# Performance work log

Hardware: AMD Instinct MI355X
Metric: run time of the kernel (lower is better)

## Reference

```python
import jax, jax.numpy as jnp
import numpy as np

N_NODES = 100000
N_EDGES = 3200000


def gcn_conv(x, edge_index, W, b, n):
    # PyG GCNConv: h = x @ W; add self-loops; symmetric deg normalization; scatter-add; + bias
    src = edge_index[0]
    dst = edge_index[1]
    loop = jnp.arange(n, dtype=src.dtype)
    src = jnp.concatenate([src, loop])
    dst = jnp.concatenate([dst, loop])
    ones = jnp.ones(src.shape[0], dtype=x.dtype)
    deg = jax.ops.segment_sum(ones, dst, num_segments=n)  # in-degree with self-loops
    dinv = jnp.where(deg > 0, jax.lax.rsqrt(deg), 0.0)
    norm = dinv[src] * dinv[dst]  # [E+N]
    h = x @ W  # [N, out]
    msg = h[src] * norm[:, None]
    out = jax.ops.segment_sum(msg, dst, num_segments=n)
    return out + b


def setup_inputs() -> dict:
    key = jax.random.key(0)
    ks = jax.random.split(key, 8)
    x = jax.random.normal(ks[0], (N_NODES, 1024), dtype=jnp.float32)
    edge_index = jax.random.randint(ks[1], (2, N_EDGES), 0, N_NODES, dtype=jnp.int32)
    def glorot(k, fan_in, fan_out):
        s = jnp.sqrt(6.0 / (fan_in + fan_out))
        return jax.random.uniform(k, (fan_in, fan_out), jnp.float32, -s, s)
    W1 = glorot(ks[2], 1024, 128)
    W2 = glorot(ks[3], 128, 128)
    W3 = glorot(ks[4], 128, 9)
    b1 = jnp.zeros((128,), jnp.float32)
    b2 = jnp.zeros((128,), jnp.float32)
    b3 = jnp.zeros((9,), jnp.float32)
    return {"x": x, "edge_index": edge_index, "W1": W1, "b1": b1, "W2": W2, "b2": b2, "W3": W3, "b3": b3}


def reference(x, edge_index, W1, b1, W2, b2, W3, b3):
    n = x.shape[0]
    h = jax.nn.relu(gcn_conv(x, edge_index, W1, b1, n))
    h = jax.nn.relu(gcn_conv(h, edge_index, W2, b2, n))
    h = gcn_conv(h, edge_index, W3, b3, n)
    return jax.nn.log_softmax(h, axis=1)
```

## Files before the change

kernel.cpp:

```cpp
#include <hip/hip_runtime.h>
#include <hip/hip_bf16.h>

typedef __attribute__((ext_vector_type(8))) short bf16x8;
typedef __attribute__((ext_vector_type(4))) float f32x4;

#define BSH 8
#define BNODES 256

__device__ __forceinline__ unsigned short f2bf(float f) {
    union { float f; unsigned int u; } x; x.f = f;
    unsigned int u = x.u;
    unsigned int r = (u + 0x7fffu + ((u >> 16) & 1u)) >> 16;
    return (unsigned short)r;
}
__device__ __forceinline__ float bf_lo(unsigned int v) { return __uint_as_float(v << 16); }
__device__ __forceinline__ float bf_hi(unsigned int v) { return __uint_as_float(v & 0xffff0000u); }

__device__ __forceinline__ void gll16(const void* g, void* l) {
    __builtin_amdgcn_global_load_lds(
        (const __attribute__((address_space(1))) unsigned int*)g,
        (__attribute__((address_space(3))) unsigned int*)l, 16, 0, 0);
}

template <int N> __device__ __forceinline__ void waitvm() {
    if constexpr (N == 0) asm volatile("s_waitcnt vmcnt(0)" ::: "memory");
    else if constexpr (N == 4) asm volatile("s_waitcnt vmcnt(4)" ::: "memory");
    else if constexpr (N == 6) asm volatile("s_waitcnt vmcnt(6)" ::: "memory");
    else if constexpr (N == 8) asm volatile("s_waitcnt vmcnt(8)" ::: "memory");
    else if constexpr (N == 12) asm volatile("s_waitcnt vmcnt(12)" ::: "memory");
    else static_assert(N == 0, "unhandled vmcnt");
}


__global__ void k_zero(int* p, int n) {
    int i = blockIdx.x * 256 + threadIdx.x;
    if (i < n) p[i] = 0;
}

__global__ __launch_bounds__(256) void kA_hist(const int* __restrict__ dst, int* bhist,
                                               int E, int nbkt) {
    __shared__ int h[512];
    for (int i = threadIdx.x; i < 512; i += 256) h[i] = 0;
    __syncthreads();
    int stride = gridDim.x * 256;
    int n4 = E >> 2;
    for (int i = blockIdx.x * 256 + threadIdx.x; i < n4; i += stride) {
        int4 d = ((const int4*)dst)[i];
        atomicAdd(&h[d.x >> BSH], 1);
        atomicAdd(&h[d.y >> BSH], 1);
        atomicAdd(&h[d.z >> BSH], 1);
        atomicAdd(&h[d.w >> BSH], 1);
    }
    for (int i = (n4 << 2) + blockIdx.x * 256 + threadIdx.x; i < E; i += stride)
        atomicAdd(&h[dst[i] >> BSH], 1);
    __syncthreads();
    for (int i = threadIdx.x; i < nbkt; i += 256)
        if (h[i]) atomicAdd(&bhist[i], h[i]);
}

__global__ void kA_scan(const int* bhist, int* bbase, int* bcur, int nbkt) {
    __shared__ int s[512];
    int t = threadIdx.x;
    int v = (t < nbkt) ? bhist[t] : 0;
    s[t] = v;
    __syncthreads();
    for (int o = 1; o < 512; o <<= 1) {
        int x = (t >= o) ? s[t - o] : 0;
        __syncthreads();
        s[t] += x;
        __syncthreads();
    }
    if (t < nbkt) { bbase[t] = s[t] - v; bcur[t] = s[t] - v; }
    if (t == nbkt - 1) bbase[nbkt] = s[t];
}

#define TPE 16
__global__ __launch_bounds__(256) void kA_scatter(const int* __restrict__ src,
                                                  const int* __restrict__ dst,
                                                  int* bcur, unsigned int* pairs,
                                                  int E, int nbkt) {
    __shared__ int hist[512];
    __shared__ int base[512];
    const int tid = threadIdx.x;
    const int t0 = blockIdx.x * (256 * TPE);
    for (int i = tid; i < 512; i += 256) hist[i] = 0;
    __syncthreads();

    int es[TPE], ed[TPE], rk[TPE];
    bool valid[TPE];
    if (t0 + 256 * TPE <= E) {
        const int4* s4 = (const int4*)(src + t0 + tid * TPE);
        const int4* d4 = (const int4*)(dst + t0 + tid * TPE);
#pragma unroll
        for (int j = 0; j < TPE / 4; j++) {
            int4 a = s4[j], b = d4[j];
            es[4 * j + 0] = a.x; es[4 * j + 1] = a.y; es[4 * j + 2] = a.z; es[4 * j + 3] = a.w;
            ed[4 * j + 0] = b.x; ed[4 * j + 1] = b.y; ed[4 * j + 2] = b.z; ed[4 * j + 3] = b.w;
            valid[4 * j + 0] = valid[4 * j + 1] = valid[4 * j + 2] = valid[4 * j + 3] = true;
        }
    } else {
#pragma unroll
        for (int j = 0; j < TPE; j++) {
            int e = t0 + tid * TPE + j;
            valid[j] = (e < E);
            es[j] = valid[j] ? src[e] : 0;
            ed[j] = valid[j] ? dst[e] : 0;
        }
    }
#pragma unroll
    for (int j = 0; j < TPE; j++)
        if (valid[j]) rk[j] = atomicAdd(&hist[ed[j] >> BSH], 1);
    __syncthreads();
    for (int i = tid; i < nbkt; i += 256) {
        int c = hist[i];
        base[i] = c ? atomicAdd(&bcur[i], c) : 0;
    }
    __syncthreads();
#pragma unroll
    for (int j = 0; j < TPE; j++) {
        if (valid[j]) {
            int b = ed[j] >> BSH;
            unsigned int p = ((unsigned int)(ed[j] & (BNODES - 1)) << 24) | (unsigned int)es[j];
            pairs[base[b] + rk[j]] = p;
        }
    }
}

__global__ __launch_bounds__(512) void kB_group(const unsigned int* __restrict__ pairs,
                                                const int* __restrict__ bbase,
                                                int* csr, int* offs, int* cnt, float* dinv,
                                                int N, int nbkt) {
    int b = blockIdx.x;
    int p0 = bbase[b], p1 = bbase[b + 1];
    int node0 = b << BSH;
    int nn = min(BNODES, N - node0);
    __shared__ int lcnt[BNODES];
    __shared__ int ss[BNODES];
    __shared__ int lcur[BNODES];
    int t = threadIdx.x;
    if (t < BNODES) lcnt[t] = 0;
    __syncthreads();
    for (int i = p0 + t; i < p1; i += 512)
        atomicAdd(&lcnt[pairs[i] >> 24], 1);
    __syncthreads();
    int v = (t < BNODES) ? lcnt[t] : 0;
    if (t < BNODES) ss[t] = v;
    __syncthreads();
    for (int o = 1; o < BNODES; o <<= 1) {
        int x = (t >= o && t < BNODES) ? ss[t - o] : 0;
        __syncthreads();
        if (t < BNODES) ss[t] += x;
        __syncthreads();
    }
    if (t < nn) {
        int o = p0 + ss[t] - v;
        offs[node0 + t] = o;
        cnt[node0 + t] = v;
        dinv[node0 + t] = rsqrtf((float)(v + 1));
        lcur[t] = o;
    }
    __syncthreads();
    for (int i = p0 + t; i < p1; i += 512) {
        unsigned int p = pairs[i];
        int pos = atomicAdd(&lcur[p >> 24], 1);
        csr[pos] = (int)(p & 0xFFFFFFu);
    }
}

__global__ void k_wt2(const float* __restrict__ W1, unsigned short* w1t,
                      const float* __restrict__ W2, unsigned short* w2t) {
    int i = blockIdx.x * 256 + threadIdx.x;
    if (i < 1024 * 128) {
        int k = i >> 7, c = i & 127;
        w1t[c * 1024 + k] = f2bf(W1[i]);
    } else {
        int j = i - 1024 * 128;
        if (j < 128 * 128) {
            int k = j >> 7, c = j & 127;
            w2t[c * 128 + k] = f2bf(W2[j]);
        }
    }
}


template <int K, bool IN_F32>
__global__ __launch_bounds__(256) void k_gemm(const void* __restrict__ Xv,
                                              const unsigned short* __restrict__ Wt,
                                              const float* __restrict__ dinv,
                                              unsigned short* __restrict__ G, int M) {
    constexpr int ABYTES = IN_F32 ? 128 * 32 * 4 : 128 * 32 * 2;
    constexpr int BBYTES = 128 * 32 * 2;
    constexpr int NT = K / 32;
    constexpr int NBUF = 3;
    constexpr int L = IN_F32 ? 6 : 4;
    static_assert(NT >= 3, "pipeline needs >=3 tiles");
    __shared__ char smem[NBUF * (ABYTES + BBYTES)];

    const int tid = threadIdx.x;
    const int m0 = blockIdx.x * 128;
    const int w = tid >> 6, l = tid & 63, r = l & 15, kg = l >> 4;
    const int wb0 = tid & ~63;

    auto stage = [&](int buf, int k0) {
        if (IN_F32) {
            const float* X = (const float*)Xv;
            char* ab = smem + buf * ABYTES;
#pragma unroll
            for (int i = 0; i < 4; i++) {
                int wb = i * 256 + wb0;
                int c = wb + l;
                int row = c >> 3, slot = c & 7;
                int srow = m0 + row; if (srow >= M) srow = M - 1;
                gll16(X + (size_t)srow * K + k0 + slot * 4, ab + (size_t)wb * 16);
            }
        } else {
            const unsigned short* X = (const unsigned short*)Xv;
            char* ab = smem + buf * ABYTES;
#pragma unroll
            for (int i = 0; i < 2; i++) {
                int wb = i * 256 + wb0;
                int c = wb + l;
                int row = c >> 2, slot = c & 3;
                int srow = m0 + row; if (srow >= M) srow = M - 1;
                gll16(X + (size_t)srow * K + k0 + slot * 8, ab + (size_t)wb * 16);
            }
        }
        {
            char* bb = smem + NBUF * ABYTES + buf * BBYTES;
#pragma unroll
            for (int i = 0; i < 2; i++) {
                int wb = i * 256 + wb0;
                int c = wb + l;
                int row = c >> 2, slot = c & 3;
                gll16(Wt + (size_t)row * K + k0 + slot * 8, bb + (size_t)wb * 16);
            }
        }
    };

    f32x4 acc[2][8];
#pragma unroll
    for (int mt = 0; mt < 2; mt++)
#pragma unroll
        for (int ct = 0; ct < 8; ct++) acc[mt][ct] = (f32x4){0.f, 0.f, 0.f, 0.f};

    auto compute = [&](int buf) {
        bf16x8 af[2], bfr[8];
        if (IN_F32) {
            const float* ab = (const float*)(smem + buf * ABYTES);
#pragma unroll
            for (int mt = 0; mt < 2; mt++) {
                int row = w * 32 + mt * 16 + r;
                float4 f0 = *(const float4*)(ab + row * 32 + kg * 8);
                float4 f1 = *(const float4*)(ab + row * 32 + kg * 8 + 4);
                union { bf16x8 v; unsigned short u[8]; } a;
                a.u[0] = f2bf(f0.x); a.u[1] = f2bf(f0.y); a.u[2] = f2bf(f0.z); a.u[3] = f2bf(f0.w);
                a.u[4] = f2bf(f1.x); a.u[5] = f2bf(f1.y); a.u[6] = f2bf(f1.z); a.u[7] = f2bf(f1.w);
                af[mt] = a.v;
            }
        } else {
            const unsigned short* ab = (const unsigned short*)(smem + buf * ABYTES);
#pragma unroll
            for (int mt = 0; mt < 2; mt++) {
                int row = w * 32 + mt * 16 + r;
                af[mt] = *(const bf16x8*)(ab + row * 32 + kg * 8);
            }
        }
        {
            const unsigned short* bb = (const unsigned short*)(smem + NBUF * ABYTES + buf * BBYTES);
#pragma unroll
            for (int ct = 0; ct < 8; ct++)
                bfr[ct] = *(const bf16x8*)(bb + (ct * 16 + r) * 32 + kg * 8);
        }
#pragma unroll
        for (int mt = 0; mt < 2; mt++)
#pragma unroll
            for (int ct = 0; ct < 8; ct++)
                acc[mt][ct] = __builtin_amdgcn_mfma_f32_16x16x32_bf16(af[mt], bfr[ct], acc[mt][ct], 0, 0, 0);
    };

    stage(0, 0);
    stage(1, 32);

    int cur = 0;
    for (int t = 0; t < NT - 2; ++t) {
        int nb = cur + 2; if (nb >= NBUF) nb -= NBUF;
        waitvm<L>();
        __builtin_amdgcn_s_barrier();
        stage(nb, (t + 2) * 32);
        compute(cur);
        cur = (cur + 1 == NBUF) ? 0 : cur + 1;
    }
    waitvm<L>();
    __builtin_amdgcn_s_barrier();
    compute(cur);
    cur = (cur + 1 == NBUF) ? 0 : cur + 1;
    waitvm<0>();
    __builtin_amdgcn_s_barrier();
    compute(cur);

#pragma unroll
    for (int mt = 0; mt < 2; mt++) {
        int rbase = m0 + w * 32 + mt * 16 + kg * 4;
        float dv[4];
#pragma unroll
        for (int q = 0; q < 4; q++) dv[q] = (rbase + q < M) ? dinv[rbase + q] : 0.f;
#pragma unroll
        for (int ct = 0; ct < 8; ct++) {
#pragma unroll
            for (int q = 0; q < 4; q++) {
                int gr = rbase + q;
                if (gr < M) G[(size_t)gr * 128 + ct * 16 + r] = f2bf(acc[mt][ct][q] * dv[q]);
            }
        }
    }
}


__global__ __launch_bounds__(256) void k_gemm3(const unsigned short* X3, const float* W3,
                                               const float* dinv, unsigned short* G3, int M) {
    __shared__ unsigned short sx[128 * 136];
    __shared__ float sw[128 * 9];
    int tid = threadIdx.x;
    int m0 = blockIdx.x * 128;
#pragma unroll
    for (int p = 0; p < 8; p++) {
        int idx = p * 256 + tid;
        int row = idx >> 4, c8 = idx & 15;
        uint4 v = make_uint4(0u, 0u, 0u, 0u);
        if (m0 + row < M) v = *(const uint4*)(X3 + (size_t)(m0 + row) * 128 + c8 * 8);
        *(uint4*)&sx[row * 136 + c8 * 8] = v;
    }
    for (int i = tid; i < 128 * 9; i += 256) sw[i] = W3[i];
    __syncthreads();

    int r = tid >> 1, h = tid & 1;
    float acc[9];
#pragma unroll
    for (int c = 0; c < 9; c++) acc[c] = 0.f;
    for (int kk = 0; kk < 64; kk++) {
        int k = h * 64 + kk;
        float xv = __uint_as_float(((unsigned int)sx[r * 136 + k]) << 16);
#pragma unroll
        for (int c = 0; c < 9; c++) acc[c] += xv * sw[k * 9 + c];
    }
#pragma unroll
    for (int c = 0; c < 9; c++) acc[c] += __shfl_xor(acc[c], 1);
    int gr = m0 + r;
    if (h == 0 && gr < M) {
        float dv = dinv[gr];
#pragma unroll
        for (int c = 0; c < 9; c++) G3[(size_t)gr * 16 + c] = f2bf(acc[c] * dv);
#pragma unroll
        for (int c = 9; c < 16; c++) G3[(size_t)gr * 16 + c] = 0;
    }
}


#define A128_CAP 1024

__global__ __launch_bounds__(256) void k_agg128(const unsigned int* __restrict__ gv,
                                                const int* __restrict__ csr,
                                                const int* __restrict__ offs,
                                                const int* __restrict__ cnt,
                                                const float* __restrict__ dinv,
                                                const float* __restrict__ bias,
                                                unsigned int* xout, int N, int do_relu) {
    __shared__ int sidx[A128_CAP];
    const int tid = threadIdx.x;
    const int n0 = blockIdx.x * 4;
    const int nlast = min(n0 + 3, N - 1);
    const int base = offs[n0];
    const int tot = offs[nlast] + cnt[nlast] - base;
    const bool lds_ok = (tot <= A128_CAP);
    if (lds_ok)
        for (int i = tid; i < tot; i += 256) sidx[i] = csr[base + i];
    __syncthreads();

    const int node = n0 + (tid >> 6);
    if (node >= N) return;
    const int l = tid & 63;
    const int ne = cnt[node];
    const int st = offs[node] - base;

    unsigned int u = gv[node * 64 + l];
    float a0 = bf_lo(u), a1 = bf_hi(u);
    int e = 0;
    if (lds_ok) {
        for (; e + 8 <= ne; e += 8) {
            int s0 = sidx[st + e], s1 = sidx[st + e + 1];
            int s2 = sidx[st + e + 2], s3 = sidx[st + e + 3];
            int s4 = sidx[st + e + 4], s5 = sidx[st + e + 5];
            int s6 = sidx[st + e + 6], s7 = sidx[st + e + 7];
            unsigned int v0 = gv[s0 * 64 + l], v1 = gv[s1 * 64 + l];
            unsigned int v2 = gv[s2 * 64 + l], v3 = gv[s3 * 64 + l];
            unsigned int v4 = gv[s4 * 64 + l], v5 = gv[s5 * 64 + l];
            unsigned int v6 = gv[s6 * 64 + l], v7 = gv[s7 * 64 + l];
            a0 += bf_lo(v0); a1 += bf_hi(v0);
            a0 += bf_lo(v1); a1 += bf_hi(v1);
            a0 += bf_lo(v2); a1 += bf_hi(v2);
            a0 += bf_lo(v3); a1 += bf_hi(v3);
            a0 += bf_lo(v4); a1 += bf_hi(v4);
            a0 += bf_lo(v5); a1 += bf_hi(v5);
            a0 += bf_lo(v6); a1 += bf_hi(v6);
            a0 += bf_lo(v7); a1 += bf_hi(v7);
        }
        for (; e < ne; e++) {
            unsigned int v = gv[sidx[st + e] * 64 + l];
            a0 += bf_lo(v); a1 += bf_hi(v);
        }
    } else {
        const int gst = offs[node];
        for (; e < ne; e++) {
            unsigned int v = gv[csr[gst + e] * 64 + l];
            a0 += bf_lo(v); a1 += bf_hi(v);
        }
    }
    float dv = dinv[node];
    float o0 = fmaf(dv, a0, bias[2 * l]);
    float o1 = fmaf(dv, a1, bias[2 * l + 1]);
    if (do_relu) { o0 = fmaxf(o0, 0.f); o1 = fmaxf(o1, 0.f); }
    xout[node * 64 + l] = (unsigned int)f2bf(o0) | ((unsigned int)f2bf(o1) << 16);
}


#define A9_CAP 3072

__global__ __launch_bounds__(256) void k_agg9(const unsigned int* __restrict__ g3v,
                                              const int* __restrict__ csr,
                                              const int* __restrict__ offs,
                                              const int* __restrict__ cnt,
                                              const float* __restrict__ dinv,
                                              const float* __restrict__ b3,
                                              float* out, int N) {
    __shared__ int sidx[A9_CAP];
    const int tid = threadIdx.x;
    const int n0 = blockIdx.x * 32;
    const int nlast = min(n0 + 31, N - 1);
    const int base = offs[n0];
    const int tot = offs[nlast] + cnt[nlast] - base;
    const bool lds_ok = (tot <= A9_CAP);
    if (lds_ok)
        for (int i = tid; i < tot; i += 256) sidx[i] = csr[base + i];
    __syncthreads();

    const int node = n0 + (tid >> 3);
    if (node >= N) return;
    const int jl = tid & 7;
    const int ne = cnt[node];

    unsigned int u = g3v[node * 8 + jl];
    float a0 = bf_lo(u), a1 = bf_hi(u);
    int e = 0;
    if (lds_ok) {
        const int st = offs[node] - base;
        for (; e + 4 <= ne; e += 4) {
            int s0 = sidx[st + e], s1 = sidx[st + e + 1];
            int s2 = sidx[st + e + 2], s3 = sidx[st + e + 3];
            unsigned int v0 = g3v[s0 * 8 + jl], v1 = g3v[s1 * 8 + jl];
            unsigned int v2 = g3v[s2 * 8 + jl], v3 = g3v[s3 * 8 + jl];
            a0 += bf_lo(v0); a1 += bf_hi(v0);
            a0 += bf_lo(v1); a1 += bf_hi(v1);
            a0 += bf_lo(v2); a1 += bf_hi(v2);
            a0 += bf_lo(v3); a1 += bf_hi(v3);
        }
        for (; e < ne; e++) {
            unsigned int v = g3v[sidx[st + e] * 8 + jl];
            a0 += bf_lo(v); a1 += bf_hi(v);
        }
    } else {
        const int gst = offs[node];
        for (; e < ne; e++) {
            unsigned int v = g3v[csr[gst + e] * 8 + jl];
            a0 += bf_lo(v); a1 += bf_hi(v);
        }
    }
    float dv = dinv[node];
    int c0 = 2 * jl, c1 = 2 * jl + 1;
    float o0 = (c0 < 9) ? fmaf(dv, a0, b3[c0]) : -INFINITY;
    float o1 = (c1 < 9) ? fmaf(dv, a1, b3[c1]) : -INFINITY;
    float m = fmaxf(o0, o1);
    for (int d = 1; d < 8; d <<= 1) m = fmaxf(m, __shfl_xor(m, d));
    float s = 0.f;
    if (c0 < 9) s += expf(o0 - m);
    if (c1 < 9) s += expf(o1 - m);
    for (int d = 1; d < 8; d <<= 1) s += __shfl_xor(s, d);
    float ls = m + logf(s);
    if (c0 < 9) out[(size_t)node * 9 + c0] = o0 - ls;
    if (c1 < 9) out[(size_t)node * 9 + c1] = o1 - ls;
}


extern "C" void kernel_launch(void* const* d_in, const int* in_sizes, int n_in,
                              void* d_out, int out_size, void* d_ws, size_t ws_size,
                              hipStream_t stream) {
    const float* x = (const float*)d_in[0];
    const int* ei = (const int*)d_in[1];
    const float* W1 = (const float*)d_in[2];
    const float* b1 = (const float*)d_in[3];
    const float* W2 = (const float*)d_in[4];
    const float* b2 = (const float*)d_in[5];
    const float* W3 = (const float*)d_in[6];
    const float* b3 = (const float*)d_in[7];
    float* out = (float*)d_out;

    const int N = in_sizes[0] / 1024;
    const int E = in_sizes[1] / 2;
    const int* src = ei;
    const int* dst = ei + E;
    const int nbkt = (N + BNODES - 1) >> BSH;

    char* ws = (char*)d_ws;
    size_t off = 0;
    auto alloc = [&](size_t bytes) -> char* {
        char* p = ws + off;
        off += (bytes + 255) & ~(size_t)255;
        return p;
    };
    int* cnt = (int*)alloc((size_t)N * 4);
    int* offs = (int*)alloc((size_t)N * 4);
    float* dinv = (float*)alloc((size_t)N * 4);
    int* bhist = (int*)alloc(520 * 4);
    int* bbase = (int*)alloc(520 * 4);
    int* bcur = (int*)alloc(520 * 4);
    unsigned int* pairs = (unsigned int*)alloc((size_t)E * 4);
    int* csr = (int*)alloc((size_t)E * 4);
    unsigned short* w1t = (unsigned short*)alloc(128 * 1024 * 2);
    unsigned short* w2t = (unsigned short*)alloc(128 * 128 * 2);
    unsigned short* gbuf = (unsigned short*)alloc((size_t)N * 128 * 2);
    unsigned short* xbuf = (unsigned short*)alloc((size_t)N * 128 * 2);
    unsigned short* g3 = (unsigned short*)alloc((size_t)N * 16 * 2);

    const int MB = (N + 127) / 128;
    const int AB = (N + 3) / 4;
    const int AB9 = (N + 31) / 32;
    const int SB = (E + 256 * TPE - 1) / (256 * TPE);
    const int WB = (1024 * 128 + 128 * 128 + 255) / 256;

    k_zero<<<3, 256, 0, stream>>>(bhist, 520);
    kA_hist<<<512, 256, 0, stream>>>(dst, bhist, E, nbkt);
    kA_scan<<<1, 512, 0, stream>>>(bhist, bbase, bcur, nbkt);
    kA_scatter<<<SB, 256, 0, stream>>>(src, dst, bcur, pairs, E, nbkt);
    kB_group<<<nbkt, 512, 0, stream>>>(pairs, bbase, csr, offs, cnt, dinv, N, nbkt);
    k_wt2<<<WB, 256, 0, stream>>>(W1, w1t, W2, w2t);

    k_gemm<1024, true><<<MB, 256, 0, stream>>>((const void*)x, w1t, dinv, gbuf, N);
    k_agg128<<<AB, 256, 0, stream>>>((const unsigned int*)gbuf, csr, offs, cnt, dinv, b1,
                                     (unsigned int*)xbuf, N, 1);
    k_gemm<128, false><<<MB, 256, 0, stream>>>((const void*)xbuf, w2t, dinv, gbuf, N);
    k_agg128<<<AB, 256, 0, stream>>>((const unsigned int*)gbuf, csr, offs, cnt, dinv, b2,
                                     (unsigned int*)xbuf, N, 1);
    k_gemm3<<<MB, 256, 0, stream>>>(xbuf, W3, dinv, g3, N);
    k_agg9<<<AB9, 256, 0, stream>>>((const unsigned int*)g3, csr, offs, cnt, dinv, b3, out, N);
}
```

Measured before the change: 500.6 us.

## Replace first-layer GEMM with per-wave register-staged fp32 load and direct weight reads

Adds a dedicated first-layer GEMM in which each wave owns 16 rows. It loads fp32 x chunks into registers, converts them to bf16 once into padded LDS, and reads the transposed W1 directly from global/L1 for the MFMA B operand. This replaces the generic 128-row LDS-pipelined kernel that converted fp32 inside the MFMA inner loop. The aim is to stream the 400MB x read more efficiently with smaller blocks and more of them. In exchange, W1 is re-read from cache by every wave, and the generic GEMM is simplified to bf16-only input.

```diff
diff --git a/kernel.cpp b/kernel.cpp
--- a/kernel.cpp
+++ b/kernel.cpp
@@ -26,8 +26,6 @@
     if constexpr (N == 0) asm volatile("s_waitcnt vmcnt(0)" ::: "memory");
     else if constexpr (N == 4) asm volatile("s_waitcnt vmcnt(4)" ::: "memory");
     else if constexpr (N == 6) asm volatile("s_waitcnt vmcnt(6)" ::: "memory");
-    else if constexpr (N == 8) asm volatile("s_waitcnt vmcnt(8)" ::: "memory");
-    else if constexpr (N == 12) asm volatile("s_waitcnt vmcnt(12)" ::: "memory");
     else static_assert(N == 0, "unhandled vmcnt");
 }
 
@@ -183,16 +181,100 @@
 }
 
 
-template <int K, bool IN_F32>
-__global__ __launch_bounds__(256) void k_gemm(const void* __restrict__ Xv,
+#define G1_RS 264
+#define G1_BUF (16 * G1_RS)
+
+__global__ __launch_bounds__(128) void k_gemm1(const float* __restrict__ X,
+                                               const unsigned short* __restrict__ Wt,
+                                               const float* __restrict__ dinv,
+                                               unsigned short* __restrict__ G, int M) {
+    __shared__ unsigned short sA[2][2][G1_BUF];
+    const int tid = threadIdx.x;
+    const int wv = tid >> 6, l = tid & 63, r = l & 15, kg = l >> 4;
+    const int m0 = blockIdx.x * 32 + wv * 16;
+    const float* Xw = X + (size_t)m0 * 1024;
+
+    f32x4 acc[8];
+#pragma unroll
+    for (int ct = 0; ct < 8; ct++) acc[ct] = (f32x4){0.f, 0.f, 0.f, 0.f};
+
+    float4 rg[16];
+
+#define G1_LOADREGS(c)                                                          \
+    {                                                                           \
+        _Pragma("unroll") for (int i = 0; i < 16; i++)                          \
+            rg[i] = *(const float4*)(Xw + i * 1024 + (c) * 256 + l * 4);        \
+    }
+
+#define G1_CVTWRITE(b)                                                          \
+    {                                                                           \
+        unsigned short* dstb = &sA[wv][(b)][0];                                 \
+        _Pragma("unroll") for (int i = 0; i < 16; i++) {                        \
+            uint2 pk;                                                           \
+            pk.x = (unsigned int)f2bf(rg[i].x) | ((unsigned int)f2bf(rg[i].y) << 16); \
+            pk.y = (unsigned int)f2bf(rg[i].z) | ((unsigned int)f2bf(rg[i].w) << 16); \
+            *(uint2*)&dstb[i * G1_RS + l * 4] = pk;                             \
+        }                                                                       \
+    }
+
+#define G1_COMPUTE(b, c)                                                        \
+    {                                                                           \
+        const unsigned short* srcb = &sA[wv][(b)][0];                           \
+        _Pragma("unroll") for (int s = 0; s < 8; s++) {                         \
+            bf16x8 af = *(const bf16x8*)&srcb[r * G1_RS + s * 32 + kg * 8];     \
+            _Pragma("unroll") for (int ct = 0; ct < 8; ct++) {                  \
+                bf16x8 bf = *(const bf16x8*)&Wt[(ct * 16 + r) * 1024 + (c) * 256 + s * 32 + kg * 8]; \
+                acc[ct] = __builtin_amdgcn_mfma_f32_16x16x32_bf16(af, bf, acc[ct], 0, 0, 0); \
+            }                                                                   \
+        }                                                                       \
+    }
+
+    G1_LOADREGS(0);
+    G1_CVTWRITE(0);
+    G1_LOADREGS(1);
+
+    G1_COMPUTE(0, 0);
+    G1_CVTWRITE(1);
+    G1_LOADREGS(2);
+
+    G1_COMPUTE(1, 1);
+    G1_CVTWRITE(0);
+    G1_LOADREGS(3);
+
+    G1_COMPUTE(0, 2);
+    G1_CVTWRITE(1);
+
+    G1_COMPUTE(1, 3);
+
+#undef G1_LOADREGS
+#undef G1_CVTWRITE
+#undef G1_COMPUTE
+
+    int rbase = m0 + kg * 4;
+    float dv[4];
+#pragma unroll
+    for (int q = 0; q < 4; q++) dv[q] = (rbase + q < M) ? dinv[rbase + q] : 0.f;
+#pragma unroll
+    for (int ct = 0; ct < 8; ct++) {
+#pragma unroll
+        for (int q = 0; q < 4; q++) {
+            int gr = rbase + q;
+            if (gr < M) G[(size_t)gr * 128 + ct * 16 + r] = f2bf(acc[ct][q] * dv[q]);
+        }
+    }
+}
+
+
+template <int K>
+__global__ __launch_bounds__(256) void k_gemm(const unsigned short* __restrict__ X,
                                               const unsigned short* __restrict__ Wt,
                                               const float* __restrict__ dinv,
                                               unsigned short* __restrict__ G, int M) {
-    constexpr int ABYTES = IN_F32 ? 128 * 32 * 4 : 128 * 32 * 2;
+    constexpr int ABYTES = 128 * 32 * 2;
     constexpr int BBYTES = 128 * 32 * 2;
     constexpr int NT = K / 32;
     constexpr int NBUF = 3;
-    constexpr int L = IN_F32 ? 6 : 4;
+    constexpr int L = 4;
     static_assert(NT >= 3, "pipeline needs >=3 tiles");
     __shared__ char smem[NBUF * (ABYTES + BBYTES)];
 
@@ -202,38 +284,22 @@
     const int wb0 = tid & ~63;
 
     auto stage = [&](int buf, int k0) {
-        if (IN_F32) {
-            const float* X = (const float*)Xv;
-            char* ab = smem + buf * ABYTES;
-#pragma unroll
-            for (int i = 0; i < 4; i++) {
-                int wb = i * 256 + wb0;
-                int c = wb + l;
-                int row = c >> 3, slot = c & 7;
-                int srow = m0 + row; if (srow >= M) srow = M - 1;
-                gll16(X + (size_t)srow * K + k0 + slot * 4, ab + (size_t)wb * 16);
-            }
-        } else {
-            const unsigned short* X = (const unsigned short*)Xv;
-            char* ab = smem + buf * ABYTES;
-#pragma unroll
-            for (int i = 0; i < 2; i++) {
-                int wb = i * 256 + wb0;
-                int c = wb + l;
-                int row = c >> 2, slot = c & 3;
-                int srow = m0 + row; if (srow >= M) srow = M - 1;
-                gll16(X + (size_t)srow * K + k0 + slot * 8, ab + (size_t)wb * 16);
-            }
-        }
-        {
-            char* bb = smem + NBUF * ABYTES + buf * BBYTES;
-#pragma unroll
-            for (int i = 0; i < 2; i++) {
-                int wb = i * 256 + wb0;
-                int c = wb + l;
-                int row = c >> 2, slot = c & 3;
-                gll16(Wt + (size_t)row * K + k0 + slot * 8, bb + (size_t)wb * 16);
-            }
+        char* ab = smem + buf * ABYTES;
+#pragma unroll
+        for (int i = 0; i < 2; i++) {
+            int wb = i * 256 + wb0;
+            int c = wb + l;
+            int row = c >> 2, slot = c & 3;
+            int srow = m0 + row; if (srow >= M) srow = M - 1;
+            gll16(X + (size_t)srow * K + k0 + slot * 8, ab + (size_t)wb * 16);
+        }
+        char* bb = smem + NBUF * ABYTES + buf * BBYTES;
+#pragma unroll
+        for (int i = 0; i < 2; i++) {
+            int wb = i * 256 + wb0;
+            int c = wb + l;
+            int row = c >> 2, slot = c & 3;
+            gll16(Wt + (size_t)row * K + k0 + slot * 8, bb + (size_t)wb * 16);
         }
     };
 
@@ -245,32 +311,16 @@
 
     auto compute = [&](int buf) {
         bf16x8 af[2], bfr[8];
-        if (IN_F32) {
-            const float* ab = (const float*)(smem + buf * ABYTES);
-#pragma unroll
-            for (int mt = 0; mt < 2; mt++) {
-                int row = w * 32 + mt * 16 + r;
-                float4 f0 = *(const float4*)(ab + row * 32 + kg * 8);
-                float4 f1 = *(const float4*)(ab + row * 32 + kg * 8 + 4);
-                union { bf16x8 v; unsigned short u[8]; } a;
-                a.u[0] = f2bf(f0.x); a.u[1] = f2bf(f0.y); a.u[2] = f2bf(f0.z); a.u[3] = f2bf(f0.w);
-                a.u[4] = f2bf(f1.x); a.u[5] = f2bf(f1.y); a.u[6] = f2bf(f1.z); a.u[7] = f2bf(f1.w);
-                af[mt] = a.v;
-            }
-        } else {
-            const unsigned short* ab = (const unsigned short*)(smem + buf * ABYTES);
-#pragma unroll
-            for (int mt = 0; mt < 2; mt++) {
-                int row = w * 32 + mt * 16 + r;
-                af[mt] = *(const bf16x8*)(ab + row * 32 + kg * 8);
-            }
-        }
-        {
-            const unsigned short* bb = (const unsigned short*)(smem + NBUF * ABYTES + buf * BBYTES);
-#pragma unroll
-            for (int ct = 0; ct < 8; ct++)
-                bfr[ct] = *(const bf16x8*)(bb + (ct * 16 + r) * 32 + kg * 8);
-        }
+        const unsigned short* ab = (const unsigned short*)(smem + buf * ABYTES);
+#pragma unroll
+        for (int mt = 0; mt < 2; mt++) {
+            int row = w * 32 + mt * 16 + r;
+            af[mt] = *(const bf16x8*)(ab + row * 32 + kg * 8);
+        }
+        const unsigned short* bb = (const unsigned short*)(smem + NBUF * ABYTES + buf * BBYTES);
+#pragma unroll
+        for (int ct = 0; ct < 8; ct++)
+            bfr[ct] = *(const bf16x8*)(bb + (ct * 16 + r) * 32 + kg * 8);
 #pragma unroll
         for (int mt = 0; mt < 2; mt++)
 #pragma unroll
@@ -530,6 +580,7 @@
     unsigned short* xbuf = (unsigned short*)alloc((size_t)N * 128 * 2);
     unsigned short* g3 = (unsigned short*)alloc((size_t)N * 16 * 2);
 
+    const int MB1 = (N + 31) / 32;
     const int MB = (N + 127) / 128;
     const int AB = (N + 3) / 4;
     const int AB9 = (N + 31) / 32;
@@ -543,10 +594,10 @@
     kB_group<<<nbkt, 512, 0, stream>>>(pairs, bbase, csr, offs, cnt, dinv, N, nbkt);
     k_wt2<<<WB, 256, 0, stream>>>(W1, w1t, W2, w2t);
 
-    k_gemm<1024, true><<<MB, 256, 0, stream>>>((const void*)x, w1t, dinv, gbuf, N);
+    k_gemm1<<<MB1, 128, 0, stream>>>(x, w1t, dinv, gbuf, N);
     k_agg128<<<AB, 256, 0, stream>>>((const unsigned int*)gbuf, csr, offs, cnt, dinv, b1,
                                      (unsigned int*)xbuf, N, 1);
-    k_gemm<128, false><<<MB, 256, 0, stream>>>((const void*)xbuf, w2t, dinv, gbuf, N);
+    k_gemm<128><<<MB, 256, 0, stream>>>(xbuf, w2t, dinv, gbuf, N);
     k_agg128<<<AB, 256, 0, stream>>>((const unsigned int*)gbuf, csr, offs, cnt, dinv, b2,
                                      (unsigned int*)xbuf, N, 1);
     k_gemm3<<<MB, 256, 0, stream>>>(xbuf, W3, dinv, g3, N);
```

Result: slower. 632.7 us (+26.4%).
